# Kernel tuning notes

Measured on AMD Instinct MI355X. Metric: run time of the kernel, lower is better.

The kernel has to match this reference:

```python
import jax, jax.numpy as jnp
import numpy as np
import math

TOTAL_HEADS = 16
CONTEXTUAL_HEADS = 4


def _compute_slopes(heads):
    def slopes_power_of_2(n):
        start = 2 ** (-2 ** (-(math.log2(n) - 3)))
        ratio = start
        return [start * ratio ** i for i in range(n)]
    if math.log2(heads).is_integer():
        return slopes_power_of_2(heads)
    closest = 2 ** math.floor(math.log2(heads))
    return slopes_power_of_2(closest) + slopes_power_of_2(2 * closest)[0::2][: heads - closest]


def setup_inputs() -> dict:
    key = jax.random.key(0)
    kq, kk = jax.random.split(key)
    b, h, s, d = 1, 16, 2048, 64
    q = jax.random.normal(kq, (b, h, s, d), dtype=jnp.float32)
    k = jax.random.normal(kk, (b, h, s, d), dtype=jnp.float32)
    cross_attn_bias = jnp.zeros((TOTAL_HEADS, 1, 1), dtype=jnp.float32)
    return {"q": q, "k": k, "cross_attn_bias": cross_attn_bias,
            "i": s, "j": s, "offset": 0, "prefix": 16}


def reference(q, k, cross_attn_bias, i, j, offset, prefix):
    b = q.shape[0]
    ch = CONTEXTUAL_HEADS
    slopes = jnp.asarray(_compute_slopes(TOTAL_HEADS), dtype=jnp.float32).reshape(-1, 1, 1)  # [H,1,1]

    # base distance bias: -|j - i|, shape [i, j]
    i_arange = jnp.arange(offset, i + offset)
    j_arange = jnp.arange(j)
    bias = -jnp.abs(j_arange[None, :] - i_arange[:, None]).astype(jnp.float32)

    # contextual heads: data-dependent bias with bidirectional cumsum
    qc = q[:, :ch]
    kc = k[:, :ch]
    dots = jnp.einsum('bhid,bhjd->bhij', qc, kc) * (qc.shape[-1] ** -0.5)
    c_bias = -jax.nn.sigmoid(dots)  # [b, ch, i, j]
    upper = jnp.triu(jnp.ones((i, j), dtype=bool), offset + 1)
    lower = jnp.tril(jnp.ones((i, j), dtype=bool), offset - 1)
    c_up = jnp.cumsum(jnp.where(upper, c_bias, 0.0), axis=-1)
    c_lo = jnp.flip(jnp.cumsum(jnp.flip(jnp.where(lower, c_bias, 0.0), axis=-1), axis=-1), axis=-1)
    c_pos = c_up + c_lo  # [b, ch, i, j]

    bias_full = jnp.concatenate(
        [c_pos, jnp.broadcast_to(bias, (b, TOTAL_HEADS - ch, i, j))], axis=1)  # [b, H, i, j]

    attn_bias = slopes * bias_full  # symmetric path

    # prefix cross-attention bias
    is_prefix = jnp.arange(j) < prefix
    is_cross = (is_prefix[:, None] ^ is_prefix[None, :])[offset:]  # [i, j]
    attn_bias = jnp.where(is_cross, cross_attn_bias, attn_bias)
    return attn_bias
```

## Files before the change

kernel.cpp:

```cpp
#include <hip/hip_runtime.h>
#include <hip/hip_bf16.h>

typedef __bf16 bf16_t;
typedef bf16_t bf16x8 __attribute__((ext_vector_type(8)));
typedef float f32x4 __attribute__((ext_vector_type(4)));

#define TH 16
#define CH 4
#define DD 64
#define SJ 2048
#define SP (SJ + 4)
#define CTXB (SJ/16)
#define NCTX (CH*CTXB)
#define AROWS 48
#define NALIBI ((TH-CH)*SJ/AROWS)
#define NBLK (NCTX + NALIBI)
#define WSK_BYTES ((size_t)CH*CTXB*2*64*16)

__device__ __forceinline__ float sigmoidf_(float x) {
    return __builtin_amdgcn_rcpf(1.0f + __expf(-x));
}

__device__ __forceinline__ float bsel(unsigned long long u, int e) {
    return __uint_as_float((((unsigned int)(u >> (16 * e)) & 0xffffu) << 16));
}

__global__ __launch_bounds__(256) void prep_kernel(
    const float* __restrict__ k, bf16_t* __restrict__ wsk)
{
    const int t    = (int)blockIdx.x * 256 + (int)threadIdx.x;
    const int h    = t >> 14;
    const int ct   = (t >> 7) & 127;
    const int kk   = (t >> 6) & 1;
    const int lane = t & 63;
    const int col  = ct * 16 + (lane & 15);
    const int db   = kk * 32 + (lane >> 4) * 8;
    const float* p = k + ((size_t)h * SJ + col) * DD + db;
    f32x4 v0 = *(const f32x4*)p;
    f32x4 v1 = *(const f32x4*)(p + 4);
    bf16x8 o;
    #pragma unroll
    for (int e = 0; e < 4; ++e) { o[e] = (bf16_t)v0[e]; o[e + 4] = (bf16_t)v1[e]; }
    *(bf16x8*)(wsk + (size_t)t * 8) = o;
}

__global__ __launch_bounds__(512, 4) void fused_kernel(
    const float* __restrict__ q, const float* __restrict__ k,
    const bf16_t* __restrict__ wsk, int use_ws,
    const float* __restrict__ cab, const int* __restrict__ offp,
    const int* __restrict__ prep, float* __restrict__ out)
{
    __shared__ bf16_t Smb[16][SP];
    __shared__ float tot[16][8];
    __shared__ float pd_in[16], pd_ex[16];
    const int tid  = (int)threadIdx.x;
    const int lane = tid & 63;
    const int w    = tid >> 6;
    const int offset = offp[0];
    const int prefix = prep[0];
    const int bx   = (int)blockIdx.x;
    const int xcd  = bx & 7;
    const int slot = bx >> 3;

    if ((slot & 1) == 0) {
        const int id = xcd * 64 + (slot >> 1);
        const int h  = id >> 7;
        const int r0 = (id & (CTXB - 1)) << 4;
        const float* qh = q + (size_t)h * SJ * DD;
        const float* kh = k + (size_t)h * SJ * DD;

        bf16x8 afrag[2];
        {
            const int row   = r0 + (lane & 15);
            const int dbase = (lane >> 4) * 8;
            const float* qp = qh + (size_t)row * DD + dbase;
            #pragma unroll
            for (int kk = 0; kk < 2; ++kk) {
                f32x4 v0 = *(const f32x4*)(qp + kk * 32);
                f32x4 v1 = *(const f32x4*)(qp + kk * 32 + 4);
                #pragma unroll
                for (int e = 0; e < 4; ++e) {
                    afrag[kk][e]     = (bf16_t)v0[e];
                    afrag[kk][e + 4] = (bf16_t)v1[e];
                }
            }
        }
        if (tid < 16) { pd_in[tid] = 0.f; pd_ex[tid] = 0.f; }
        for (int t = 0; t < 16; ++t) {
            const int c0 = w * 256 + t * 16;
            f32x4 acc = {0.f, 0.f, 0.f, 0.f};
            if (use_ws) {
                const size_t fb = (((size_t)h * CTXB + (c0 >> 4)) * 2) * 64 + lane;
                #pragma unroll
                for (int kk = 0; kk < 2; ++kk) {
                    bf16x8 bfrag = *(const bf16x8*)(wsk + (fb + (size_t)kk * 64) * 8);
                    acc = __builtin_amdgcn_mfma_f32_16x16x32_bf16(afrag[kk], bfrag, acc, 0, 0, 0);
                }
            } else {
                #pragma unroll
                for (int kk = 0; kk < 2; ++kk) {
                    const int col = c0 + (lane & 15);
                    const int db  = kk * 32 + (lane >> 4) * 8;
                    const float* p = kh + (size_t)col * DD + db;
                    f32x4 v0 = *(const f32x4*)(p);
                    f32x4 v1 = *(const f32x4*)(p + 4);
                    bf16x8 bfrag;
                    #pragma unroll
                    for (int e = 0; e < 4; ++e) {
                        bfrag[e]     = (bf16_t)v0[e];
                        bfrag[e + 4] = (bf16_t)v1[e];
                    }
                    acc = __builtin_amdgcn_mfma_f32_16x16x32_bf16(afrag[kk], bfrag, acc, 0, 0, 0);
                }
            }
            const int ccol = c0 + (lane & 15);
            const int rb   = (lane >> 4) * 4;
            #pragma unroll
            for (int m = 0; m < 4; ++m)
                Smb[rb + m][ccol] = (bf16_t)sigmoidf_(acc[m] * 0.125f);
        }
        __syncthreads();

        const float slope = exp2f(-0.5f * (float)(h + 1));
        const float cabv  = cab[h];
        const int cb = w * 256 + lane * 4;
        unsigned long long u[16];
        float base_[16];
        #pragma unroll
        for (int rl = 0; rl < 16; ++rl) {
            u[rl] = *(const unsigned long long*)(&Smb[rl][cb]);
            const float i3 = ((bsel(u[rl], 0) + bsel(u[rl], 1))
                            + (bsel(u[rl], 2) + bsel(u[rl], 3)));
            float x = i3;
            #pragma unroll
            for (int d = 1; d < 64; d <<= 1) {
                float y = __shfl_up(x, d);
                if (lane >= d) x += y;
            }
            if (lane == 63) tot[rl][w] = x;
            base_[rl] = x - i3;
        }
        __syncthreads();
        #pragma unroll
        for (int rl = 0; rl < 16; ++rl) {
            float b = 0.f;
            #pragma unroll
            for (int s = 0; s < 7; ++s)
                b += (s < w) ? tot[rl][s] : 0.f;
            base_[rl] += b;
            const int rg = r0 + rl, dg = rg + offset;
            const int cin = dg < SJ ? dg : SJ - 1;
            const int cex = (dg - 1) < SJ ? dg - 1 : SJ - 1;
            if (dg >= 0 && (unsigned)(cin - cb) < 4u) {
                const int e = cin - cb;
                float pi = bsel(u[rl], 0);
                if (e > 0) pi += bsel(u[rl], 1);
                if (e > 1) pi += bsel(u[rl], 2);
                if (e > 2) pi += bsel(u[rl], 3);
                pd_in[rl] = base_[rl] + pi;
            }
            if (dg >= 1 && (unsigned)(cex - cb) < 4u) {
                const int e = cex - cb;
                float pi = bsel(u[rl], 0);
                if (e > 0) pi += bsel(u[rl], 1);
                if (e > 1) pi += bsel(u[rl], 2);
                if (e > 2) pi += bsel(u[rl], 3);
                pd_ex[rl] = base_[rl] + pi;
            }
        }
        __syncthreads();
        #pragma unroll
        for (int rl = 0; rl < 16; ++rl) {
            const int rg = r0 + rl, dg = rg + offset;
            const float pdin = pd_in[rl];
            const float pdex = pd_ex[rl];
            const bool rpre = dg < prefix;
            const float b  = base_[rl];
            const float i0 = b  + bsel(u[rl], 0);
            const float i1 = i0 + bsel(u[rl], 1);
            const float i2 = i1 + bsel(u[rl], 2);
            const float i3 = i2 + bsel(u[rl], 3);
            const float Pc[4] = {i0, i1, i2, i3};
            const float Pm[4] = {b, i0, i1, i2};
            float* orow = out + ((size_t)h * SJ + rg) * (size_t)SJ;
            f32x4 o;
            #pragma unroll
            for (int e = 0; e < 4; ++e) {
                const int c = cb + e;
                const float cpos = (c > dg) ? -(Pc[e] - pdin)
                                 : (c < dg) ? -(pdex - Pm[e]) : 0.f;
                const bool cross = (c < prefix) != rpre;
                o[e] = cross ? cabv : slope * cpos;
            }
            *(f32x4*)(orow + cb) = o;
        }
    } else {
        const int aid = xcd * 64 + (slot >> 1);
        const int R0  = aid * AROWS;
        #pragma unroll
        for (int rr = 0; rr < 6; ++rr) {
            const int R  = R0 + rr * 8 + w;
            const int h  = CH + (R >> 11);
            const int r  = R & (SJ - 1);
            const int dg = r + offset;
            const float slope = exp2f(-0.5f * (float)(h + 1));
            const float cabv  = cab[h];
            const bool rpre = dg < prefix;
            float* orow = out + ((size_t)h * SJ + r) * (size_t)SJ;
            #pragma unroll
            for (int s = 0; s < 8; ++s) {
                const int cb = s * 256 + lane * 4;
                f32x4 o;
                #pragma unroll
                for (int e = 0; e < 4; ++e) {
                    const int c = cb + e;
                    const float v = -fabsf((float)(c - dg)) * slope;
                    const bool cross = (c < prefix) != rpre;
                    o[e] = cross ? cabv : v;
                }
                *(f32x4*)(orow + cb) = o;
            }
        }
    }
}

extern "C" void kernel_launch(void* const* d_in, const int* in_sizes, int n_in,
                              void* d_out, int out_size, void* d_ws, size_t ws_size,
                              hipStream_t stream) {
    const float* q    = (const float*)d_in[0];
    const float* k    = (const float*)d_in[1];
    const float* cab  = (const float*)d_in[2];
    const int*   offp = (const int*)d_in[5];
    const int*   prep = (const int*)d_in[6];
    float* out = (float*)d_out;
    bf16_t* wsk = (bf16_t*)d_ws;

    const int use_ws = (ws_size >= WSK_BYTES) ? 1 : 0;
    if (use_ws)
        prep_kernel<<<dim3(256), dim3(256), 0, stream>>>(k, wsk);
    fused_kernel<<<dim3(NBLK), dim3(512), 0, stream>>>(q, k, wsk, use_ws,
                                                       cab, offp, prep, out);
}
```

Before: 73.09 us.

## Split fused kernel into separate ALiBi and contextual-head kernels

```diff
diff --git a/kernel.cpp b/kernel.cpp
--- a/kernel.cpp
+++ b/kernel.cpp
@@ -4,6 +4,7 @@
 typedef __bf16 bf16_t;
 typedef bf16_t bf16x8 __attribute__((ext_vector_type(8)));
 typedef float f32x4 __attribute__((ext_vector_type(4)));
+typedef unsigned long long u64_t;
 
 #define TH 16
 #define CH 4
@@ -12,16 +13,15 @@
 #define SP (SJ + 4)
 #define CTXB (SJ/16)
 #define NCTX (CH*CTXB)
-#define AROWS 48
-#define NALIBI ((TH-CH)*SJ/AROWS)
-#define NBLK (NCTX + NALIBI)
+#define ABLK_ROWS 24
+#define NALIBI ((TH-CH)*SJ/ABLK_ROWS)
 #define WSK_BYTES ((size_t)CH*CTXB*2*64*16)
 
 __device__ __forceinline__ float sigmoidf_(float x) {
     return __builtin_amdgcn_rcpf(1.0f + __expf(-x));
 }
 
-__device__ __forceinline__ float bsel(unsigned long long u, int e) {
+__device__ __forceinline__ float bsel(u64_t u, int e) {
     return __uint_as_float((((unsigned int)(u >> (16 * e)) & 0xffffu) << 16));
 }
 
@@ -44,7 +44,42 @@
     *(bf16x8*)(wsk + (size_t)t * 8) = o;
 }
 
-__global__ __launch_bounds__(512, 4) void fused_kernel(
+__global__ __launch_bounds__(512) void alibi_kernel(
+    const float* __restrict__ cab, const int* __restrict__ offp,
+    const int* __restrict__ prep, float* __restrict__ out)
+{
+    const int lane = (int)threadIdx.x & 63;
+    const int w    = (int)threadIdx.x >> 6;
+    const int offset = offp[0];
+    const int prefix = prep[0];
+    const int R0 = (int)blockIdx.x * ABLK_ROWS;
+    #pragma unroll
+    for (int rr = 0; rr < 3; ++rr) {
+        const int R  = R0 + rr * 8 + w;
+        const int h  = CH + (R >> 11);
+        const int r  = R & (SJ - 1);
+        const int dg = r + offset;
+        const float slope = exp2f(-0.5f * (float)(h + 1));
+        const float cabv  = cab[h];
+        const bool rpre = dg < prefix;
+        float* orow = out + ((size_t)h * SJ + r) * (size_t)SJ;
+        #pragma unroll
+        for (int s = 0; s < 8; ++s) {
+            const int cb = s * 256 + lane * 4;
+            f32x4 o;
+            #pragma unroll
+            for (int e = 0; e < 4; ++e) {
+                const int c = cb + e;
+                const float v = -fabsf((float)(c - dg)) * slope;
+                const bool cross = (c < prefix) != rpre;
+                o[e] = cross ? cabv : v;
+            }
+            *(f32x4*)(orow + cb) = o;
+        }
+    }
+}
+
+__global__ __launch_bounds__(512, 2) void ctx_kernel(
     const float* __restrict__ q, const float* __restrict__ k,
     const bf16_t* __restrict__ wsk, int use_ws,
     const float* __restrict__ cab, const int* __restrict__ offp,
@@ -58,169 +93,136 @@
     const int w    = tid >> 6;
     const int offset = offp[0];
     const int prefix = prep[0];
-    const int bx   = (int)blockIdx.x;
-    const int xcd  = bx & 7;
-    const int slot = bx >> 3;
-
-    if ((slot & 1) == 0) {
-        const int id = xcd * 64 + (slot >> 1);
-        const int h  = id >> 7;
-        const int r0 = (id & (CTXB - 1)) << 4;
-        const float* qh = q + (size_t)h * SJ * DD;
-        const float* kh = k + (size_t)h * SJ * DD;
-
-        bf16x8 afrag[2];
-        {
-            const int row   = r0 + (lane & 15);
-            const int dbase = (lane >> 4) * 8;
-            const float* qp = qh + (size_t)row * DD + dbase;
+    const int id = (int)blockIdx.x;
+    const int h  = id >> 7;
+    const int r0 = (id & (CTXB - 1)) << 4;
+    const float* qh = q + (size_t)h * SJ * DD;
+    const float* kh = k + (size_t)h * SJ * DD;
+
+    bf16x8 afrag[2];
+    {
+        const int row   = r0 + (lane & 15);
+        const int dbase = (lane >> 4) * 8;
+        const float* qp = qh + (size_t)row * DD + dbase;
+        #pragma unroll
+        for (int kk = 0; kk < 2; ++kk) {
+            f32x4 v0 = *(const f32x4*)(qp + kk * 32);
+            f32x4 v1 = *(const f32x4*)(qp + kk * 32 + 4);
+            #pragma unroll
+            for (int e = 0; e < 4; ++e) {
+                afrag[kk][e]     = (bf16_t)v0[e];
+                afrag[kk][e + 4] = (bf16_t)v1[e];
+            }
+        }
+    }
+    if (tid < 16) { pd_in[tid] = 0.f; pd_ex[tid] = 0.f; }
+    for (int t = 0; t < 16; ++t) {
+        const int c0 = w * 256 + t * 16;
+        f32x4 acc = {0.f, 0.f, 0.f, 0.f};
+        if (use_ws) {
+            const size_t fb = (((size_t)h * CTXB + (c0 >> 4)) * 2) * 64 + lane;
             #pragma unroll
             for (int kk = 0; kk < 2; ++kk) {
-                f32x4 v0 = *(const f32x4*)(qp + kk * 32);
-                f32x4 v1 = *(const f32x4*)(qp + kk * 32 + 4);
+                bf16x8 bfrag = *(const bf16x8*)(wsk + (fb + (size_t)kk * 64) * 8);
+                acc = __builtin_amdgcn_mfma_f32_16x16x32_bf16(afrag[kk], bfrag, acc, 0, 0, 0);
+            }
+        } else {
+            #pragma unroll
+            for (int kk = 0; kk < 2; ++kk) {
+                const int col = c0 + (lane & 15);
+                const int db  = kk * 32 + (lane >> 4) * 8;
+                const float* p = kh + (size_t)col * DD + db;
+                f32x4 v0 = *(const f32x4*)(p);
+                f32x4 v1 = *(const f32x4*)(p + 4);
+                bf16x8 bfrag;
                 #pragma unroll
                 for (int e = 0; e < 4; ++e) {
-                    afrag[kk][e]     = (bf16_t)v0[e];
-                    afrag[kk][e + 4] = (bf16_t)v1[e];
+                    bfrag[e]     = (bf16_t)v0[e];
+                    bfrag[e + 4] = (bf16_t)v1[e];
                 }
-            }
-        }
-        if (tid < 16) { pd_in[tid] = 0.f; pd_ex[tid] = 0.f; }
-        for (int t = 0; t < 16; ++t) {
-            const int c0 = w * 256 + t * 16;
-            f32x4 acc = {0.f, 0.f, 0.f, 0.f};
-            if (use_ws) {
-                const size_t fb = (((size_t)h * CTXB + (c0 >> 4)) * 2) * 64 + lane;
-                #pragma unroll
-                for (int kk = 0; kk < 2; ++kk) {
-                    bf16x8 bfrag = *(const bf16x8*)(wsk + (fb + (size_t)kk * 64) * 8);
-                    acc = __builtin_amdgcn_mfma_f32_16x16x32_bf16(afrag[kk], bfrag, acc, 0, 0, 0);
-                }
-            } else {
-                #pragma unroll
-                for (int kk = 0; kk < 2; ++kk) {
-                    const int col = c0 + (lane & 15);
-                    const int db  = kk * 32 + (lane >> 4) * 8;
-                    const float* p = kh + (size_t)col * DD + db;
-                    f32x4 v0 = *(const f32x4*)(p);
-                    f32x4 v1 = *(const f32x4*)(p + 4);
-                    bf16x8 bfrag;
-                    #pragma unroll
-                    for (int e = 0; e < 4; ++e) {
-                        bfrag[e]     = (bf16_t)v0[e];
-                        bfrag[e + 4] = (bf16_t)v1[e];
-                    }
-                    acc = __builtin_amdgcn_mfma_f32_16x16x32_bf16(afrag[kk], bfrag, acc, 0, 0, 0);
-                }
-            }
-            const int ccol = c0 + (lane & 15);
-            const int rb   = (lane >> 4) * 4;
-            #pragma unroll
-            for (int m = 0; m < 4; ++m)
-                Smb[rb + m][ccol] = (bf16_t)sigmoidf_(acc[m] * 0.125f);
-        }
-        __syncthreads();
-
-        const float slope = exp2f(-0.5f * (float)(h + 1));
-        const float cabv  = cab[h];
-        const int cb = w * 256 + lane * 4;
-        unsigned long long u[16];
-        float base_[16];
-        #pragma unroll
-        for (int rl = 0; rl < 16; ++rl) {
-            u[rl] = *(const unsigned long long*)(&Smb[rl][cb]);
-            const float i3 = ((bsel(u[rl], 0) + bsel(u[rl], 1))
-                            + (bsel(u[rl], 2) + bsel(u[rl], 3)));
-            float x = i3;
-            #pragma unroll
-            for (int d = 1; d < 64; d <<= 1) {
-                float y = __shfl_up(x, d);
-                if (lane >= d) x += y;
-            }
-            if (lane == 63) tot[rl][w] = x;
-            base_[rl] = x - i3;
-        }
-        __syncthreads();
-        #pragma unroll
-        for (int rl = 0; rl < 16; ++rl) {
-            float b = 0.f;
-            #pragma unroll
-            for (int s = 0; s < 7; ++s)
-                b += (s < w) ? tot[rl][s] : 0.f;
-            base_[rl] += b;
-            const int rg = r0 + rl, dg = rg + offset;
-            const int cin = dg < SJ ? dg : SJ - 1;
-            const int cex = (dg - 1) < SJ ? dg - 1 : SJ - 1;
-            if (dg >= 0 && (unsigned)(cin - cb) < 4u) {
-                const int e = cin - cb;
-                float pi = bsel(u[rl], 0);
-                if (e > 0) pi += bsel(u[rl], 1);
-                if (e > 1) pi += bsel(u[rl], 2);
-                if (e > 2) pi += bsel(u[rl], 3);
-                pd_in[rl] = base_[rl] + pi;
-            }
-            if (dg >= 1 && (unsigned)(cex - cb) < 4u) {
-                const int e = cex - cb;
-                float pi = bsel(u[rl], 0);
-                if (e > 0) pi += bsel(u[rl], 1);
-                if (e > 1) pi += bsel(u[rl], 2);
-                if (e > 2) pi += bsel(u[rl], 3);
-                pd_ex[rl] = base_[rl] + pi;
-            }
-        }
-        __syncthreads();
-        #pragma unroll
-        for (int rl = 0; rl < 16; ++rl) {
-            const int rg = r0 + rl, dg = rg + offset;
-            const float pdin = pd_in[rl];
-            const float pdex = pd_ex[rl];
-            const bool rpre = dg < prefix;
-            const float b  = base_[rl];
-            const float i0 = b  + bsel(u[rl], 0);
-            const float i1 = i0 + bsel(u[rl], 1);
-            const float i2 = i1 + bsel(u[rl], 2);
-            const float i3 = i2 + bsel(u[rl], 3);
-            const float Pc[4] = {i0, i1, i2, i3};
-            const float Pm[4] = {b, i0, i1, i2};
-            float* orow = out + ((size_t)h * SJ + rg) * (size_t)SJ;
-            f32x4 o;
-            #pragma unroll
-            for (int e = 0; e < 4; ++e) {
-                const int c = cb + e;
-                const float cpos = (c > dg) ? -(Pc[e] - pdin)
-                                 : (c < dg) ? -(pdex - Pm[e]) : 0.f;
-                const bool cross = (c < prefix) != rpre;
-                o[e] = cross ? cabv : slope * cpos;
-            }
-            *(f32x4*)(orow + cb) = o;
-        }
-    } else {
-        const int aid = xcd * 64 + (slot >> 1);
-        const int R0  = aid * AROWS;
-        #pragma unroll
-        for (int rr = 0; rr < 6; ++rr) {
-            const int R  = R0 + rr * 8 + w;
-            const int h  = CH + (R >> 11);
-            const int r  = R & (SJ - 1);
-            const int dg = r + offset;
-            const float slope = exp2f(-0.5f * (float)(h + 1));
-            const float cabv  = cab[h];
-            const bool rpre = dg < prefix;
-            float* orow = out + ((size_t)h * SJ + r) * (size_t)SJ;
-            #pragma unroll
-            for (int s = 0; s < 8; ++s) {
-                const int cb = s * 256 + lane * 4;
-                f32x4 o;
-                #pragma unroll
-                for (int e = 0; e < 4; ++e) {
-                    const int c = cb + e;
-                    const float v = -fabsf((float)(c - dg)) * slope;
-                    const bool cross = (c < prefix) != rpre;
-                    o[e] = cross ? cabv : v;
-                }
-                *(f32x4*)(orow + cb) = o;
-            }
-        }
+                acc = __builtin_amdgcn_mfma_f32_16x16x32_bf16(afrag[kk], bfrag, acc, 0, 0, 0);
+            }
+        }
+        const int ccol = c0 + (lane & 15);
+        const int rb   = (lane >> 4) * 4;
+        #pragma unroll
+        for (int m = 0; m < 4; ++m)
+            Smb[rb + m][ccol] = (bf16_t)sigmoidf_(acc[m] * 0.125f);
+    }
+    __syncthreads();
+
+    const float slope = exp2f(-0.5f * (float)(h + 1));
+    const float cabv  = cab[h];
+    const int cb = w * 256 + lane * 4;
+    unsigned long long u[16];
+    float base_[16];
+    #pragma unroll
+    for (int rl = 0; rl < 16; ++rl) {
+        u[rl] = *(const u64_t*)(&Smb[rl][cb]);
+        const float i3 = ((bsel(u[rl], 0) + bsel(u[rl], 1))
+                        + (bsel(u[rl], 2) + bsel(u[rl], 3)));
+        float x = i3;
+        #pragma unroll
+        for (int d = 1; d < 64; d <<= 1) {
+            float y = __shfl_up(x, d);
+            if (lane >= d) x += y;
+        }
+        if (lane == 63) tot[rl][w] = x;
+        base_[rl] = x - i3;
+    }
+    __syncthreads();
+    #pragma unroll
+    for (int rl = 0; rl < 16; ++rl) {
+        float b = 0.f;
+        #pragma unroll
+        for (int s = 0; s < 7; ++s)
+            b += (s < w) ? tot[rl][s] : 0.f;
+        base_[rl] += b;
+        const int rg = r0 + rl, dg = rg + offset;
+        const int cin = dg < SJ ? dg : SJ - 1;
+        const int cex = (dg - 1) < SJ ? dg - 1 : SJ - 1;
+        if (dg >= 0 && (unsigned)(cin - cb) < 4u) {
+            const int e = cin - cb;
+            float pi = bsel(u[rl], 0);
+            if (e > 0) pi += bsel(u[rl], 1);
+            if (e > 1) pi += bsel(u[rl], 2);
+            if (e > 2) pi += bsel(u[rl], 3);
+            pd_in[rl] = base_[rl] + pi;
+        }
+        if (dg >= 1 && (unsigned)(cex - cb) < 4u) {
+            const int e = cex - cb;
+            float pi = bsel(u[rl], 0);
+            if (e > 0) pi += bsel(u[rl], 1);
+            if (e > 1) pi += bsel(u[rl], 2);
+            if (e > 2) pi += bsel(u[rl], 3);
+            pd_ex[rl] = base_[rl] + pi;
+        }
+    }
+    __syncthreads();
+    #pragma unroll
+    for (int rl = 0; rl < 16; ++rl) {
+        const int rg = r0 + rl, dg = rg + offset;
+        const float pdin = pd_in[rl];
+        const float pdex = pd_ex[rl];
+        const bool rpre = dg < prefix;
+        const float b  = base_[rl];
+        const float i0 = b  + bsel(u[rl], 0);
+        const float i1 = i0 + bsel(u[rl], 1);
+        const float i2 = i1 + bsel(u[rl], 2);
+        const float i3 = i2 + bsel(u[rl], 3);
+        const float Pc[4] = {i0, i1, i2, i3};
+        const float Pm[4] = {b, i0, i1, i2};
+        float* orow = out + ((size_t)h * SJ + rg) * (size_t)SJ;
+        f32x4 o;
+        #pragma unroll
+        for (int e = 0; e < 4; ++e) {
+            const int c = cb + e;
+            const float cpos = (c > dg) ? -(Pc[e] - pdin)
+                             : (c < dg) ? -(pdex - Pm[e]) : 0.f;
+            const bool cross = (c < prefix) != rpre;
+            o[e] = cross ? cabv : slope * cpos;
+        }
+        *(f32x4*)(orow + cb) = o;
     }
 }
 
@@ -238,6 +240,7 @@
     const int use_ws = (ws_size >= WSK_BYTES) ? 1 : 0;
     if (use_ws)
         prep_kernel<<<dim3(256), dim3(256), 0, stream>>>(k, wsk);
-    fused_kernel<<<dim3(NBLK), dim3(512), 0, stream>>>(q, k, wsk, use_ws,
-                                                       cab, offp, prep, out);
-}
+    alibi_kernel<<<dim3(NALIBI), dim3(512), 0, stream>>>(cab, offp, prep, out);
+    ctx_kernel<<<dim3(NCTX), dim3(512), 0, stream>>>(q, k, wsk, use_ws,
+                                                     cab, offp, prep, out);
+}
```

After: 79.70 us. 1.09x slower.

## Shrink contextual row tiles to 8 rows and interleave ALiBi blocks 2:3

Applied to the files above, without the earlier changes.

```diff
diff --git a/kernel.cpp b/kernel.cpp
--- a/kernel.cpp
+++ b/kernel.cpp
@@ -4,24 +4,26 @@
 typedef __bf16 bf16_t;
 typedef bf16_t bf16x8 __attribute__((ext_vector_type(8)));
 typedef float f32x4 __attribute__((ext_vector_type(4)));
+typedef unsigned long long u64_t;
 
 #define TH 16
 #define CH 4
 #define DD 64
 #define SJ 2048
 #define SP (SJ + 4)
-#define CTXB (SJ/16)
-#define NCTX (CH*CTXB)
-#define AROWS 48
+#define RROWS 8
+#define KT (SJ/16)
+#define NCTX (CH*SJ/RROWS)
+#define AROWS 16
 #define NALIBI ((TH-CH)*SJ/AROWS)
 #define NBLK (NCTX + NALIBI)
-#define WSK_BYTES ((size_t)CH*CTXB*2*64*16)
+#define WSK_BYTES ((size_t)CH*KT*2*64*16)
 
 __device__ __forceinline__ float sigmoidf_(float x) {
     return __builtin_amdgcn_rcpf(1.0f + __expf(-x));
 }
 
-__device__ __forceinline__ float bsel(unsigned long long u, int e) {
+__device__ __forceinline__ float bsel(u64_t u, int e) {
     return __uint_as_float((((unsigned int)(u >> (16 * e)) & 0xffffu) << 16));
 }
 
@@ -50,28 +52,27 @@
     const float* __restrict__ cab, const int* __restrict__ offp,
     const int* __restrict__ prep, float* __restrict__ out)
 {
-    __shared__ bf16_t Smb[16][SP];
-    __shared__ float tot[16][8];
-    __shared__ float pd_in[16], pd_ex[16];
+    __shared__ bf16_t Smb[RROWS][SP];
+    __shared__ float tot[RROWS][8];
+    __shared__ float pd_in[RROWS], pd_ex[RROWS];
     const int tid  = (int)threadIdx.x;
     const int lane = tid & 63;
     const int w    = tid >> 6;
     const int offset = offp[0];
     const int prefix = prep[0];
-    const int bx   = (int)blockIdx.x;
-    const int xcd  = bx & 7;
-    const int slot = bx >> 3;
-
-    if ((slot & 1) == 0) {
-        const int id = xcd * 64 + (slot >> 1);
-        const int h  = id >> 7;
-        const int r0 = (id & (CTXB - 1)) << 4;
+    const int bx = (int)blockIdx.x;
+    const int m5 = bx % 5;
+
+    if (m5 < 2) {
+        const int id = (bx / 5) * 2 + m5;
+        const int h  = id >> 8;
+        const int r0 = (id & 255) * RROWS;
         const float* qh = q + (size_t)h * SJ * DD;
         const float* kh = k + (size_t)h * SJ * DD;
 
         bf16x8 afrag[2];
         {
-            const int row   = r0 + (lane & 15);
+            const int row   = r0 + ((lane & 15) & 7);
             const int dbase = (lane >> 4) * 8;
             const float* qp = qh + (size_t)row * DD + dbase;
             #pragma unroll
@@ -85,12 +86,13 @@
                 }
             }
         }
-        if (tid < 16) { pd_in[tid] = 0.f; pd_ex[tid] = 0.f; }
+        if (tid < RROWS) { pd_in[tid] = 0.f; pd_ex[tid] = 0.f; }
+        const int rb = (lane >> 4) * 4;
         for (int t = 0; t < 16; ++t) {
             const int c0 = w * 256 + t * 16;
             f32x4 acc = {0.f, 0.f, 0.f, 0.f};
             if (use_ws) {
-                const size_t fb = (((size_t)h * CTXB + (c0 >> 4)) * 2) * 64 + lane;
+                const size_t fb = (((size_t)h * KT + (c0 >> 4)) * 2) * 64 + lane;
                 #pragma unroll
                 for (int kk = 0; kk < 2; ++kk) {
                     bf16x8 bfrag = *(const bf16x8*)(wsk + (fb + (size_t)kk * 64) * 8);
@@ -113,22 +115,23 @@
                     acc = __builtin_amdgcn_mfma_f32_16x16x32_bf16(afrag[kk], bfrag, acc, 0, 0, 0);
                 }
             }
-            const int ccol = c0 + (lane & 15);
-            const int rb   = (lane >> 4) * 4;
-            #pragma unroll
-            for (int m = 0; m < 4; ++m)
-                Smb[rb + m][ccol] = (bf16_t)sigmoidf_(acc[m] * 0.125f);
+            if (rb < RROWS) {
+                const int ccol = c0 + (lane & 15);
+                #pragma unroll
+                for (int m = 0; m < 4; ++m)
+                    Smb[rb + m][ccol] = (bf16_t)sigmoidf_(acc[m] * 0.125f);
+            }
         }
         __syncthreads();
 
         const float slope = exp2f(-0.5f * (float)(h + 1));
         const float cabv  = cab[h];
         const int cb = w * 256 + lane * 4;
-        unsigned long long u[16];
-        float base_[16];
-        #pragma unroll
-        for (int rl = 0; rl < 16; ++rl) {
-            u[rl] = *(const unsigned long long*)(&Smb[rl][cb]);
+        u64_t u[RROWS];
+        float base_[RROWS];
+        #pragma unroll
+        for (int rl = 0; rl < RROWS; ++rl) {
+            u[rl] = *(const u64_t*)(&Smb[rl][cb]);
             const float i3 = ((bsel(u[rl], 0) + bsel(u[rl], 1))
                             + (bsel(u[rl], 2) + bsel(u[rl], 3)));
             float x = i3;
@@ -142,7 +145,7 @@
         }
         __syncthreads();
         #pragma unroll
-        for (int rl = 0; rl < 16; ++rl) {
+        for (int rl = 0; rl < RROWS; ++rl) {
             float b = 0.f;
             #pragma unroll
             for (int s = 0; s < 7; ++s)
@@ -170,7 +173,7 @@
         }
         __syncthreads();
         #pragma unroll
-        for (int rl = 0; rl < 16; ++rl) {
+        for (int rl = 0; rl < RROWS; ++rl) {
             const int rg = r0 + rl, dg = rg + offset;
             const float pdin = pd_in[rl];
             const float pdex = pd_ex[rl];
@@ -195,18 +198,17 @@
             *(f32x4*)(orow + cb) = o;
         }
     } else {
-        const int aid = xcd * 64 + (slot >> 1);
-        const int R0  = aid * AROWS;
-        #pragma unroll
-        for (int rr = 0; rr < 6; ++rr) {
-            const int R  = R0 + rr * 8 + w;
-            const int h  = CH + (R >> 11);
-            const int r  = R & (SJ - 1);
-            const int dg = r + offset;
-            const float slope = exp2f(-0.5f * (float)(h + 1));
-            const float cabv  = cab[h];
+        const int id = (bx / 5) * 3 + (m5 - 2);
+        const int h  = CH + (id >> 7);
+        const int r0 = (id & 127) * AROWS;
+        const float slope = exp2f(-0.5f * (float)(h + 1));
+        const float cabv  = cab[h];
+        #pragma unroll
+        for (int rr = 0; rr < 2; ++rr) {
+            const int rg = r0 + rr * 8 + w;
+            const int dg = rg + offset;
             const bool rpre = dg < prefix;
-            float* orow = out + ((size_t)h * SJ + r) * (size_t)SJ;
+            float* orow = out + ((size_t)h * SJ + rg) * (size_t)SJ;
             #pragma unroll
             for (int s = 0; s < 8; ++s) {
                 const int cb = s * 256 + lane * 4;
```

Result: faster. 61.81 us (-15.4%).
